# Optimization experiments

Hardware: AMD Instinct MI355X
Metric: run time of the kernel (lower is better)

## Reference

```python
import jax, jax.numpy as jnp
import numpy as np

GROUPS = 32
HEADS = 8
EPS = 1e-5


def setup_inputs() -> dict:
    key = jax.random.key(0)
    k1, k2 = jax.random.split(key)
    B, C, H, W = 8, 512, 32, 32
    x = jax.random.normal(k1, (B, C, H, W), dtype=jnp.float32)
    gn_weight = jnp.ones((C,), dtype=jnp.float32)
    gn_bias = jnp.zeros((C,), dtype=jnp.float32)
    w1 = jax.random.normal(k2, (3 * C, C, 1), dtype=jnp.float32) * (C ** -0.5)
    b1 = jnp.zeros((3 * C,), dtype=jnp.float32)
    return {"x": x, "gn_weight": gn_weight, "gn_bias": gn_bias, "w1": w1, "b1": b1}


def reference(x, gn_weight, gn_bias, w1, b1):
    B, C, H, W = x.shape
    T = H * W
    ch = C // HEADS
    # GroupNorm over (C/G, H, W) per group
    xg = x.reshape(B, GROUPS, -1)
    mu = jnp.mean(xg, axis=-1, keepdims=True)
    var = jnp.var(xg, axis=-1, keepdims=True)
    xn = ((xg - mu) * jax.lax.rsqrt(var + EPS)).reshape(B, C, T)
    xn = xn * gn_weight[:, None] + gn_bias[:, None]
    # 1x1 Conv1d -> QKV: [B, 3C, T]
    qkv = jnp.einsum('oc,bct->bot', w1[:, :, 0], xn) + b1[:, None]
    q, k, v = jnp.split(qkv, 3, axis=1)
    q = q.reshape(B, HEADS, ch, T)
    k = k.reshape(B, HEADS, ch, T)
    v = v.reshape(B, HEADS, ch, T)
    scale = ch ** -0.25  # applied to both q and k, per guided-diffusion QKVAttention
    w = jnp.einsum('bhct,bhcs->bhts', q * scale, k * scale)  # [B,H,T,T]
    w = jax.nn.softmax(w, axis=-1)
    a = jnp.einsum('bhts,bhcs->bhct', w, v).reshape(B, C, H, W)
    return a + x
```

## Files before the change

### kernel.cpp

```cpp
#include <hip/hip_runtime.h>
#include <hip/hip_bf16.h>

#define NB 8
#define NC 512
#define NT 1024
#define NHEADS 8
#define NCH 64
#define NGROUPS 32
#define NGC 16

typedef __attribute__((ext_vector_type(4))) unsigned short u16x4;
typedef __attribute__((ext_vector_type(8))) unsigned short u16x8;
typedef __attribute__((ext_vector_type(4))) float f32x4;
typedef __attribute__((ext_vector_type(8))) __bf16 bfv8;

static __device__ __forceinline__ unsigned short f2bf(float f) {
    __bf16 h = (__bf16)f;
    return __builtin_bit_cast(unsigned short, h);
}

static __device__ __forceinline__ f32x4 mfma_bf16(u16x8 a, u16x8 b, f32x4 c) {
    return __builtin_amdgcn_mfma_f32_16x16x32_bf16(
        __builtin_bit_cast(bfv8, a), __builtin_bit_cast(bfv8, b), c, 0, 0, 0);
}

static __device__ __forceinline__ void gl_lds16(const unsigned short* g, unsigned short* l) {
    __builtin_amdgcn_global_load_lds(
        (const __attribute__((address_space(1))) unsigned int*)g,
        (__attribute__((address_space(3))) unsigned int*)l, 16, 0, 0);
}

__global__ __launch_bounds__(512) void k_gn_w1(const float* __restrict__ x,
                                               const float* __restrict__ gw,
                                               const float* __restrict__ gb,
                                               const float* __restrict__ w1,
                                               unsigned short* __restrict__ xnT,
                                               unsigned short* __restrict__ w1b) {
    int tid = threadIdx.x;
    if (blockIdx.x >= 256) {
        int i = ((blockIdx.x - 256) * 512 + tid) * 8;
        f32x4 a = *(const f32x4*)(w1 + i);
        f32x4 b = *(const f32x4*)(w1 + i + 4);
        u16x8 o;
#pragma unroll
        for (int j = 0; j < 4; ++j) { o[j] = f2bf(a[j]); o[4 + j] = f2bf(b[j]); }
        *(u16x8*)(w1b + i) = o;
        return;
    }
    int b = blockIdx.x >> 5, g = blockIdx.x & 31;
    int half = tid >> 8, tl = tid & 255;
    int t4 = tl * 4;
    const float* xb = x + ((size_t)(b * NC + g * NGC + half * 8)) * NT;

    f32x4 vv[8];
    float s = 0.f, ss = 0.f;
#pragma unroll
    for (int cc = 0; cc < 8; ++cc) {
        f32x4 v = *(const f32x4*)(xb + cc * NT + t4);
        vv[cc] = v;
#pragma unroll
        for (int i = 0; i < 4; ++i) { s += v[i]; ss += v[i] * v[i]; }
    }
#pragma unroll
    for (int off = 1; off < 64; off <<= 1) { s += __shfl_xor(s, off); ss += __shfl_xor(ss, off); }
    __shared__ float rs_[8], rss[8];
    int w = tid >> 6;
    if ((tid & 63) == 0) { rs_[w] = s; rss[w] = ss; }
    __syncthreads();
    s = 0.f; ss = 0.f;
#pragma unroll
    for (int i = 0; i < 8; ++i) { s += rs_[i]; ss += rss[i]; }
    float mu  = s * (1.f / 16384.f);
    float var = ss * (1.f / 16384.f) - mu * mu;
    float rstd = rsqrtf(var + 1e-5f);

    float wgt[8], bia[8];
#pragma unroll
    for (int cc = 0; cc < 8; ++cc) {
        float ww = gw[g * NGC + half * 8 + cc] * rstd;
        wgt[cc] = ww;
        bia[cc] = gb[g * NGC + half * 8 + cc] - mu * ww;
    }
#pragma unroll
    for (int i = 0; i < 4; ++i) {
        unsigned short o[8];
#pragma unroll
        for (int cc = 0; cc < 8; ++cc) o[cc] = f2bf(vv[cc][i] * wgt[cc] + bia[cc]);
        unsigned short* dst = xnT + ((size_t)(b * NT + t4 + i)) * NC + g * NGC + half * 8;
        *(u16x8*)dst = *(u16x8*)o;
    }
}

__global__ __launch_bounds__(256) void k_qkv_gemm(const unsigned short* __restrict__ w1b,
                                                  const unsigned short* __restrict__ xnT,
                                                  const float* __restrict__ b1,
                                                  unsigned short* __restrict__ q_t,
                                                  unsigned short* __restrict__ k_t,
                                                  unsigned short* __restrict__ vbuf) {
    __shared__ unsigned short As[2 * 128 * 64];
    __shared__ unsigned short Bs[2 * 128 * 64];
    int bid = blockIdx.x;
    int lbid = (bid & 7) * 96 + (bid >> 3);
    int bb = lbid / 96;
    int rr_ = lbid % 96;
    int tm = rr_ >> 3, tn = rr_ & 7;
    int tid = threadIdx.x;
    int l = tid & 63, w = tid >> 6;
    int wm = w >> 1, wn = w & 1;
    int ll = l & 15, lg = l >> 4;
    int rl = l >> 3, sl = l & 7;
    int ssl = sl ^ rl;

    const unsigned short* Ag = w1b + (size_t)(tm * 128) * NC;
    const unsigned short* Bg = xnT + (size_t)(bb * NT + tn * 128) * NC;

    auto STAGE = [&](int k0, int buf) {
        unsigned short* dA = As + buf * 8192 + w * 32 * 64;
        unsigned short* dB = Bs + buf * 8192 + w * 32 * 64;
#pragma unroll
        for (int i = 0; i < 4; ++i) {
            int row = w * 32 + i * 8 + rl;
            gl_lds16(Ag + (size_t)row * NC + k0 + ssl * 8, dA + i * 512);
            gl_lds16(Bg + (size_t)row * NC + k0 + ssl * 8, dB + i * 512);
        }
    };

    f32x4 acc[4][4] = {};
    STAGE(0, 0);
    __syncthreads();
    int cur = 0;
    for (int ks = 0; ks < 8; ++ks) {
        if (ks < 7) STAGE((ks + 1) * 64, cur ^ 1);
        const char* Ac = (const char*)(As + cur * 8192);
        const char* Bc = (const char*)(Bs + cur * 8192);
#pragma unroll
        for (int kk = 0; kk < 2; ++kk) {
            u16x8 af[4], bf[4];
#pragma unroll
            for (int m = 0; m < 4; ++m) {
                int row = wm * 64 + m * 16 + ll;
                af[m] = *(const u16x8*)(Ac + row * 128 + ((kk * 64 + lg * 16) ^ ((row & 7) << 4)));
            }
#pragma unroll
            for (int n = 0; n < 4; ++n) {
                int row = wn * 64 + n * 16 + ll;
                bf[n] = *(const u16x8*)(Bc + row * 128 + ((kk * 64 + lg * 16) ^ ((row & 7) << 4)));
            }
#pragma unroll
            for (int m = 0; m < 4; ++m)
#pragma unroll
                for (int n = 0; n < 4; ++n)
                    acc[m][n] = mfma_bf16(af[m], bf[n], acc[m][n]);
        }
        __syncthreads();
        cur ^= 1;
    }

    if (tm < 8) {
        int qk = tm >> 2;
        int h = (tm & 3) * 2 + wm;
        float sc = qk ? 1.f : 0.125f * 1.44269504088896f;
        int obase = tm * 128 + wm * 64;
        unsigned short* dst = (qk ? k_t : q_t) + ((size_t)(bb * 8 + h)) * NT * NCH;
#pragma unroll
        for (int m = 0; m < 4; ++m) {
#pragma unroll
            for (int n = 0; n < 4; ++n) {
                int t = tn * 128 + wn * 64 + n * 16 + ll;
                u16x4 pk;
#pragma unroll
                for (int r = 0; r < 4; ++r)
                    pk[r] = f2bf((acc[m][n][r] + b1[obase + m * 16 + lg * 4 + r]) * sc);
                *(u16x4*)(dst + (size_t)t * NCH + m * 16 + lg * 4) = pk;
            }
        }
    } else {
        int vcb = (tm - 8) * 128 + wm * 64;
#pragma unroll
        for (int m = 0; m < 4; ++m)
#pragma unroll
            for (int r = 0; r < 4; ++r) {
                int vc = vcb + m * 16 + lg * 4 + r;
                float bias = b1[1024 + vc];
#pragma unroll
                for (int n = 0; n < 4; ++n) {
                    int t = tn * 128 + wn * 64 + n * 16 + ll;
                    vbuf[(size_t)(bb * NC + vc) * NT + t] = f2bf(acc[m][n][r] + bias);
                }
            }
    }
}

#define SW1B(r) (((r) & 7) << 4)
__global__ __launch_bounds__(256) void k_attn(const unsigned short* __restrict__ q_t,
                                              const unsigned short* __restrict__ k_t,
                                              const unsigned short* __restrict__ vbuf,
                                              const float* __restrict__ x,
                                              float* __restrict__ out) {
    __shared__ unsigned char smem[65536];
    unsigned short* sK = (unsigned short*)smem;
    unsigned short* sV = (unsigned short*)(smem + 24576);
    unsigned short* sP = (unsigned short*)(smem + 49152);

    int lbid = ((blockIdx.x & 7) << 6) | (blockIdx.x >> 3);
    int b  = lbid >> 6;
    int h  = (lbid >> 3) & 7;
    int qt = lbid & 7;
    int t0 = qt * 128;

    int tid = threadIdx.x;
    int l = tid & 63, w = tid >> 6;
    int ll = l & 15, lg = l >> 4;
    int rl = l >> 3, sl = l & 7;
    int ssl = sl ^ rl;

    const unsigned short* Qg = q_t + ((size_t)((b * 8 + h) * NT + t0 + w * 32)) * NCH;
    const unsigned short* Kg = k_t + ((size_t)(b * 8 + h)) * NT * NCH;
    const unsigned short* Vg = vbuf + ((size_t)(b * NC + h * NCH)) * NT;

    u16x8 aq[2][2];
#pragma unroll
    for (int m = 0; m < 2; ++m)
#pragma unroll
        for (int kk = 0; kk < 2; ++kk)
            aq[m][kk] = *(const u16x8*)(Qg + (m * 16 + ll) * NCH + kk * 32 + lg * 8);

    f32x4 acc_o[2][4] = {};
    float rs[2] = {};

    auto STAGE = [&](int s0, int buf) {
        unsigned short* dK = sK + buf * 4096 + w * 1024;
        unsigned short* dV = sV + buf * 4096 + w * 1024;
#pragma unroll
        for (int i = 0; i < 2; ++i) {
            int row = w * 16 + i * 8 + rl;
            gl_lds16(Kg + (size_t)(s0 + row) * NCH + ssl * 8, dK + i * 512);
            gl_lds16(Vg + (size_t)row * NT + s0 + ssl * 8, dV + i * 512);
        }
    };

    STAGE(0, 0);
    STAGE(64, 1);
    STAGE(128, 2);

    char* sPw = (char*)(sP + w * 2048);
    for (int tile = 0; tile < 16; ++tile) {
        if (tile < 14)       asm volatile("s_waitcnt vmcnt(8)" ::: "memory");
        else if (tile == 14) asm volatile("s_waitcnt vmcnt(4)" ::: "memory");
        else                 asm volatile("s_waitcnt vmcnt(0)" ::: "memory");
        __builtin_amdgcn_s_barrier();
        __builtin_amdgcn_sched_barrier(0);

        int cur = tile % 3;
        const char* Kc = (const char*)(sK + cur * 4096);
        const char* Vc = (const char*)(sV + cur * 4096);

        f32x4 sc_[2][4];
#pragma unroll
        for (int j = 0; j < 4; ++j) {
            int row = j * 16 + ll;
            int sw = SW1B(row);
            u16x8 b0 = *(const u16x8*)(Kc + row * 128 + ((lg * 16) ^ sw));
            u16x8 b1v = *(const u16x8*)(Kc + row * 128 + ((64 + lg * 16) ^ sw));
            f32x4 z = {0.f, 0.f, 0.f, 0.f};
            sc_[0][j] = mfma_bf16(b1v, aq[0][1], mfma_bf16(b0, aq[0][0], z));
            sc_[1][j] = mfma_bf16(b1v, aq[1][1], mfma_bf16(b0, aq[1][0], z));
        }

#pragma unroll
        for (int m = 0; m < 2; ++m) {
            int t = m * 16 + ll;
            int sw = (t & 7) << 4;
#pragma unroll
            for (int j = 0; j < 4; ++j) {
                float p0 = __builtin_amdgcn_exp2f(sc_[m][j][0]);
                float p1 = __builtin_amdgcn_exp2f(sc_[m][j][1]);
                float p2 = __builtin_amdgcn_exp2f(sc_[m][j][2]);
                float p3 = __builtin_amdgcn_exp2f(sc_[m][j][3]);
                rs[m] += (p0 + p1) + (p2 + p3);
                u16x4 pk = {f2bf(p0), f2bf(p1), f2bf(p2), f2bf(p3)};
                *(u16x4*)(sPw + t * 128 + ((j * 32 + lg * 8) ^ sw)) = pk;
            }
        }

        u16x8 ap[2][2];
#pragma unroll
        for (int m = 0; m < 2; ++m) {
            int t = m * 16 + ll;
            int sw = (t & 7) << 4;
#pragma unroll
            for (int kk = 0; kk < 2; ++kk)
                ap[m][kk] = *(const u16x8*)(sPw + t * 128 + ((kk * 64 + lg * 16) ^ sw));
        }
#pragma unroll
        for (int n = 0; n < 4; ++n) {
            int row = n * 16 + ll;
            int sw = SW1B(row);
#pragma unroll
            for (int kk = 0; kk < 2; ++kk) {
                u16x8 bv = *(const u16x8*)(Vc + row * 128 + ((kk * 64 + lg * 16) ^ sw));
                acc_o[0][n] = mfma_bf16(ap[0][kk], bv, acc_o[0][n]);
                acc_o[1][n] = mfma_bf16(ap[1][kk], bv, acc_o[1][n]);
            }
        }

        __builtin_amdgcn_sched_barrier(0);
        __builtin_amdgcn_s_barrier();
        if (tile < 13) STAGE((tile + 3) * 64, cur);
    }

    float rinv[2][4];
#pragma unroll
    for (int m = 0; m < 2; ++m) {
        float s = rs[m];
        s += __shfl_xor(s, 16);
        s += __shfl_xor(s, 32);
#pragma unroll
        for (int r = 0; r < 4; ++r)
            rinv[m][r] = 1.f / __shfl(s, (l & 48) + lg * 4 + r);
    }

    char* sO = (char*)(smem + w * 8192);
#pragma unroll
    for (int m = 0; m < 2; ++m)
#pragma unroll
        for (int n = 0; n < 4; ++n) {
            int c = n * 16 + ll;
            f32x4 o4;
#pragma unroll
            for (int r = 0; r < 4; ++r) o4[r] = acc_o[m][n][r] * rinv[m][r];
            *(f32x4*)(sO + c * 128 + ((m * 64 + lg * 16) ^ SW1B(c))) = o4;
        }
#pragma unroll
    for (int i2 = 0; i2 < 8; ++i2) {
        int c = i2 * 8 + rl;
        f32x4 o4 = *(const f32x4*)(sO + c * 128 + ((sl * 16) ^ SW1B(c)));
        size_t gidx = ((size_t)(b * NC + h * NCH + c)) * NT + t0 + w * 32 + sl * 4;
        f32x4 xv = *(const f32x4*)(x + gidx);
#pragma unroll
        for (int q = 0; q < 4; ++q) o4[q] += xv[q];
        *(f32x4*)(out + gidx) = o4;
    }
}

extern "C" void kernel_launch(void* const* d_in, const int* in_sizes, int n_in,
                              void* d_out, int out_size, void* d_ws, size_t ws_size,
                              hipStream_t stream) {
    (void)in_sizes; (void)n_in; (void)out_size; (void)ws_size;
    const float* x  = (const float*)d_in[0];
    const float* gw = (const float*)d_in[1];
    const float* gb = (const float*)d_in[2];
    const float* w1 = (const float*)d_in[3];
    const float* b1 = (const float*)d_in[4];
    float* out = (float*)d_out;

    char* ws = (char*)d_ws;
    unsigned short* w1b  = (unsigned short*)(ws);
    unsigned short* xnT  = (unsigned short*)(ws + (size_t)(2u << 20));
    unsigned short* q_t  = (unsigned short*)(ws + (size_t)(11u << 20));
    unsigned short* k_t  = (unsigned short*)(ws + (size_t)(20u << 20));
    unsigned short* vbuf = (unsigned short*)(ws + (size_t)(29u << 20));

    k_gn_w1<<<dim3(448), dim3(512), 0, stream>>>(x, gw, gb, w1, xnT, w1b);
    k_qkv_gemm<<<dim3(768), dim3(256), 0, stream>>>(w1b, xnT, b1, q_t, k_t, vbuf);
    k_attn<<<dim3(512), dim3(256), 0, stream>>>(q_t, k_t, vbuf, x, out);
}
```

Before: 65.69 us.

## Switch attention to 32x32 MFMA with in-register P via permlane swap

Rewrites the attention inner loop to use 32x32x16 bf16 MFMA tiles instead of 16x16x32. The softmax probabilities are packed with v_cvt_pk_bf16_f32 and rearranged into the PV A-operand layout with v_permlane32_swap, so the per-tile LDS round trip for P goes away. This shrinks shared memory to 48KB and adds a launch bound of 3 blocks per CU to raise occupancy. The main risk is register pressure from 16-wide accumulators under the tighter launch bound, plus getting the lane mapping of the swapped P fragments right.

```diff
diff --git a/kernel.cpp b/kernel.cpp
--- a/kernel.cpp
+++ b/kernel.cpp
@@ -12,6 +12,7 @@
 typedef __attribute__((ext_vector_type(4))) unsigned short u16x4;
 typedef __attribute__((ext_vector_type(8))) unsigned short u16x8;
 typedef __attribute__((ext_vector_type(4))) float f32x4;
+typedef __attribute__((ext_vector_type(16))) float f32x16;
 typedef __attribute__((ext_vector_type(8))) __bf16 bfv8;
 
 static __device__ __forceinline__ unsigned short f2bf(float f) {
@@ -19,8 +20,19 @@
     return __builtin_bit_cast(unsigned short, h);
 }
 
+static __device__ __forceinline__ unsigned cvtpk(float lo, float hi) {
+    unsigned r;
+    asm("v_cvt_pk_bf16_f32 %0, %1, %2" : "=v"(r) : "v"(lo), "v"(hi));
+    return r;
+}
+
 static __device__ __forceinline__ f32x4 mfma_bf16(u16x8 a, u16x8 b, f32x4 c) {
     return __builtin_amdgcn_mfma_f32_16x16x32_bf16(
+        __builtin_bit_cast(bfv8, a), __builtin_bit_cast(bfv8, b), c, 0, 0, 0);
+}
+
+static __device__ __forceinline__ f32x16 mfma32(u16x8 a, u16x8 b, f32x16 c) {
+    return __builtin_amdgcn_mfma_f32_32x32x16_bf16(
         __builtin_bit_cast(bfv8, a), __builtin_bit_cast(bfv8, b), c, 0, 0, 0);
 }
 
@@ -191,16 +203,14 @@
     }
 }
 
-#define SW1B(r) (((r) & 7) << 4)
-__global__ __launch_bounds__(256) void k_attn(const unsigned short* __restrict__ q_t,
-                                              const unsigned short* __restrict__ k_t,
-                                              const unsigned short* __restrict__ vbuf,
-                                              const float* __restrict__ x,
-                                              float* __restrict__ out) {
-    __shared__ unsigned char smem[65536];
+__global__ __launch_bounds__(256, 3) void k_attn(const unsigned short* __restrict__ q_t,
+                                                 const unsigned short* __restrict__ k_t,
+                                                 const unsigned short* __restrict__ vbuf,
+                                                 const float* __restrict__ x,
+                                                 float* __restrict__ out) {
+    __shared__ unsigned char smem[49152];
     unsigned short* sK = (unsigned short*)smem;
     unsigned short* sV = (unsigned short*)(smem + 24576);
-    unsigned short* sP = (unsigned short*)(smem + 49152);
 
     int lbid = ((blockIdx.x & 7) << 6) | (blockIdx.x >> 3);
     int b  = lbid >> 6;
@@ -210,7 +220,7 @@
 
     int tid = threadIdx.x;
     int l = tid & 63, w = tid >> 6;
-    int ll = l & 15, lg = l >> 4;
+    int lh = l & 31, hi = l >> 5;
     int rl = l >> 3, sl = l & 7;
     int ssl = sl ^ rl;
 
@@ -218,15 +228,13 @@
     const unsigned short* Kg = k_t + ((size_t)(b * 8 + h)) * NT * NCH;
     const unsigned short* Vg = vbuf + ((size_t)(b * NC + h * NCH)) * NT;
 
-    u16x8 aq[2][2];
-#pragma unroll
-    for (int m = 0; m < 2; ++m)
-#pragma unroll
-        for (int kk = 0; kk < 2; ++kk)
-            aq[m][kk] = *(const u16x8*)(Qg + (m * 16 + ll) * NCH + kk * 32 + lg * 8);
-
-    f32x4 acc_o[2][4] = {};
-    float rs[2] = {};
+    u16x8 aq[4];
+#pragma unroll
+    for (int ks = 0; ks < 4; ++ks)
+        aq[ks] = *(const u16x8*)(Qg + lh * NCH + ks * 16 + hi * 8);
+
+    f32x16 acc_o[2] = {};
+    float rs = 0.f;
 
     auto STAGE = [&](int s0, int buf) {
         unsigned short* dK = sK + buf * 4096 + w * 1024;
@@ -243,7 +251,6 @@
     STAGE(64, 1);
     STAGE(128, 2);
 
-    char* sPw = (char*)(sP + w * 2048);
     for (int tile = 0; tile < 16; ++tile) {
         if (tile < 14)       asm volatile("s_waitcnt vmcnt(8)" ::: "memory");
         else if (tile == 14) asm volatile("s_waitcnt vmcnt(4)" ::: "memory");
@@ -255,52 +262,38 @@
         const char* Kc = (const char*)(sK + cur * 4096);
         const char* Vc = (const char*)(sV + cur * 4096);
 
-        f32x4 sc_[2][4];
-#pragma unroll
-        for (int j = 0; j < 4; ++j) {
-            int row = j * 16 + ll;
-            int sw = SW1B(row);
-            u16x8 b0 = *(const u16x8*)(Kc + row * 128 + ((lg * 16) ^ sw));
-            u16x8 b1v = *(const u16x8*)(Kc + row * 128 + ((64 + lg * 16) ^ sw));
-            f32x4 z = {0.f, 0.f, 0.f, 0.f};
-            sc_[0][j] = mfma_bf16(b1v, aq[0][1], mfma_bf16(b0, aq[0][0], z));
-            sc_[1][j] = mfma_bf16(b1v, aq[1][1], mfma_bf16(b0, aq[1][0], z));
-        }
-
-#pragma unroll
-        for (int m = 0; m < 2; ++m) {
-            int t = m * 16 + ll;
-            int sw = (t & 7) << 4;
-#pragma unroll
-            for (int j = 0; j < 4; ++j) {
-                float p0 = __builtin_amdgcn_exp2f(sc_[m][j][0]);
-                float p1 = __builtin_amdgcn_exp2f(sc_[m][j][1]);
-                float p2 = __builtin_amdgcn_exp2f(sc_[m][j][2]);
-                float p3 = __builtin_amdgcn_exp2f(sc_[m][j][3]);
-                rs[m] += (p0 + p1) + (p2 + p3);
-                u16x4 pk = {f2bf(p0), f2bf(p1), f2bf(p2), f2bf(p3)};
-                *(u16x4*)(sPw + t * 128 + ((j * 32 + lg * 8) ^ sw)) = pk;
-            }
-        }
-
-        u16x8 ap[2][2];
-#pragma unroll
-        for (int m = 0; m < 2; ++m) {
-            int t = m * 16 + ll;
-            int sw = (t & 7) << 4;
-#pragma unroll
-            for (int kk = 0; kk < 2; ++kk)
-                ap[m][kk] = *(const u16x8*)(sPw + t * 128 + ((kk * 64 + lg * 16) ^ sw));
-        }
-#pragma unroll
-        for (int n = 0; n < 4; ++n) {
-            int row = n * 16 + ll;
-            int sw = SW1B(row);
-#pragma unroll
-            for (int kk = 0; kk < 2; ++kk) {
-                u16x8 bv = *(const u16x8*)(Vc + row * 128 + ((kk * 64 + lg * 16) ^ sw));
-                acc_o[0][n] = mfma_bf16(ap[0][kk], bv, acc_o[0][n]);
-                acc_o[1][n] = mfma_bf16(ap[1][kk], bv, acc_o[1][n]);
+#pragma unroll
+        for (int jt = 0; jt < 2; ++jt) {
+            f32x16 sc = {};
+#pragma unroll
+            for (int ks = 0; ks < 4; ++ks) {
+                int row = jt * 32 + lh;
+                u16x8 kf = *(const u16x8*)(Kc + row * 128 + ((ks * 32 + hi * 16) ^ ((row & 7) << 4)));
+                sc = mfma32(kf, aq[ks], sc);
+            }
+            float p[16];
+#pragma unroll
+            for (int r = 0; r < 16; ++r) {
+                p[r] = __builtin_amdgcn_exp2f(sc[r]);
+                rs += p[r];
+            }
+#pragma unroll
+            for (int eo = 0; eo < 2; ++eo) {
+                unsigned A0 = cvtpk(p[8 * eo + 0], p[8 * eo + 1]);
+                unsigned A1 = cvtpk(p[8 * eo + 2], p[8 * eo + 3]);
+                unsigned B0 = cvtpk(p[8 * eo + 4], p[8 * eo + 5]);
+                unsigned B1 = cvtpk(p[8 * eo + 6], p[8 * eo + 7]);
+                asm("v_permlane32_swap_b32 %0, %1" : "+v"(A0), "+v"(B0));
+                asm("v_permlane32_swap_b32 %0, %1" : "+v"(A1), "+v"(B1));
+                union { unsigned u[4]; u16x8 v; } ap_;
+                ap_.u[0] = A0; ap_.u[1] = A1; ap_.u[2] = B0; ap_.u[3] = B1;
+                int kt = jt * 2 + eo;
+#pragma unroll
+                for (int ct = 0; ct < 2; ++ct) {
+                    int crow = ct * 32 + lh;
+                    u16x8 vf = *(const u16x8*)(Vc + crow * 128 + ((kt * 32 + hi * 16) ^ ((crow & 7) << 4)));
+                    acc_o[ct] = mfma32(ap_.v, vf, acc_o[ct]);
+                }
             }
         }
 
@@ -309,32 +302,29 @@
         if (tile < 13) STAGE((tile + 3) * 64, cur);
     }
 
-    float rinv[2][4];
-#pragma unroll
-    for (int m = 0; m < 2; ++m) {
-        float s = rs[m];
-        s += __shfl_xor(s, 16);
-        s += __shfl_xor(s, 32);
-#pragma unroll
-        for (int r = 0; r < 4; ++r)
-            rinv[m][r] = 1.f / __shfl(s, (l & 48) + lg * 4 + r);
-    }
+    float full = rs + __shfl_xor(rs, 32);
+    float rinv[16];
+#pragma unroll
+    for (int reg = 0; reg < 16; ++reg)
+        rinv[reg] = 1.f / __shfl(full, (reg & 3) + 8 * (reg >> 2) + 4 * hi);
 
     char* sO = (char*)(smem + w * 8192);
 #pragma unroll
-    for (int m = 0; m < 2; ++m)
-#pragma unroll
-        for (int n = 0; n < 4; ++n) {
-            int c = n * 16 + ll;
+    for (int ct = 0; ct < 2; ++ct) {
+        int c = ct * 32 + lh;
+        int swz = (c & 7) << 4;
+#pragma unroll
+        for (int q = 0; q < 4; ++q) {
             f32x4 o4;
 #pragma unroll
-            for (int r = 0; r < 4; ++r) o4[r] = acc_o[m][n][r] * rinv[m][r];
-            *(f32x4*)(sO + c * 128 + ((m * 64 + lg * 16) ^ SW1B(c))) = o4;
-        }
+            for (int r = 0; r < 4; ++r) o4[r] = acc_o[ct][q * 4 + r] * rinv[q * 4 + r];
+            *(f32x4*)(sO + c * 128 + ((q * 32 + hi * 16) ^ swz)) = o4;
+        }
+    }
 #pragma unroll
     for (int i2 = 0; i2 < 8; ++i2) {
         int c = i2 * 8 + rl;
-        f32x4 o4 = *(const f32x4*)(sO + c * 128 + ((sl * 16) ^ SW1B(c)));
+        f32x4 o4 = *(const f32x4*)(sO + c * 128 + ((sl * 16) ^ ((c & 7) << 4)));
         size_t gidx = ((size_t)(b * NC + h * NCH + c)) * NT + t0 + w * 32 + sl * 4;
         f32x4 xv = *(const f32x4*)(x + gidx);
 #pragma unroll
```

After: 63.29 us. -3.6%, faster.
